# Performance work log

Measured on AMD Instinct MI355X. Metric: run time of the kernel, lower is better.

## Reference

```python
import jax, jax.numpy as jnp
import numpy as np

N_EXPERTS = 16
D_IN = 2048
D_OUT = 2048
BATCH = 4096


def setup_inputs() -> dict:
    key = jax.random.key(0)
    k_x, k_m, k_a, k_w, k_b = jax.random.split(key, 5)
    xs = jax.random.normal(k_x, (BATCH, D_IN), dtype=jnp.float32)
    mxs = jax.random.normal(k_m, (BATCH,), dtype=jnp.float32)
    actions = jax.random.randint(k_a, (BATCH,), 0, N_EXPERTS, dtype=jnp.int64)
    # Per-expert Linear params: W[e] is [d_out, d_in], b[e] is [d_out]
    scale = 1.0 / np.sqrt(D_IN)
    W = jax.random.uniform(k_w, (N_EXPERTS, D_OUT, D_IN), dtype=jnp.float32,
                           minval=-scale, maxval=scale)
    b = jax.random.uniform(k_b, (N_EXPERTS, D_OUT), dtype=jnp.float32,
                           minval=-scale, maxval=scale)
    return {"xs": xs, "mxs": mxs, "actions": actions, "W": W, "b": b}


def reference(xs, mxs, actions, W, b):
    # Original: per-sample dispatch y[i] = submodule[actions[i]](x[i]).
    # Grouped form: for each expert e, run the full-batch GEMM and combine
    # with a mask (fixed small loop over experts; no data-dim Python loop).
    ys = jnp.zeros((xs.shape[0], W.shape[1]), dtype=xs.dtype)
    for e in range(W.shape[0]):
        ye = xs @ W[e].T + b[e]                      # [B, d_out]
        mask = (actions == e)[:, None]               # [B, 1]
        ys = jnp.where(mask, ye, ys)
    return (ys, mxs, actions)
```

## Files before the change

kernel.cpp:

```cpp
#include <hip/hip_runtime.h>
#include <hip/hip_bf16.h>

#define BATCH 4096
#define NEXP  16
#define DIN   2048
#define DOUT  2048

#define BM 128
#define BN 64
#define NKT 64
#define NPAIR 32

#define WS_X_OFF   65536
#define PADROWS    4352
#define WS_X_BYTES ((size_t)PADROWS * 4096)

typedef __attribute__((ext_vector_type(4))) float f32x4;
typedef __attribute__((ext_vector_type(8))) short bf16x8;

__global__ void sort_kernel(const int* __restrict__ actions,
                            const float* __restrict__ mxs,
                            float* __restrict__ out_tail,
                            int* __restrict__ offs,
                            int* __restrict__ poffs,
                            int* __restrict__ sorted) {
    __shared__ int s_cnt[NEXP];
    __shared__ int s_cur[NEXP];
    const int tid = threadIdx.x;
    if (tid < NEXP) s_cnt[tid] = 0;
    __syncthreads();
    for (int i = tid; i < BATCH; i += blockDim.x) {
        int a = actions[i];
        atomicAdd(&s_cnt[a], 1);
        out_tail[i] = mxs[i];
        out_tail[BATCH + i] = (float)a;
    }
    __syncthreads();
    if (tid == 0) {
        int run = 0, prun = 0;
        for (int e = 0; e < NEXP; ++e) {
            offs[e] = run;  s_cur[e] = run;
            poffs[e] = prun;
            run += s_cnt[e];
            prun += (s_cnt[e] + 15) & ~15;
        }
        offs[NEXP] = run;
        poffs[NEXP] = prun;
    }
    __syncthreads();
    for (int i = tid; i < BATCH; i += blockDim.x) {
        int e = actions[i];
        int pos = atomicAdd(&s_cur[e], 1);
        sorted[pos] = i;
    }
}

__device__ __forceinline__ unsigned rne2(float x0, float x1) {
    unsigned b0 = __float_as_uint(x0), b1 = __float_as_uint(x1);
    b0 = b0 + 0x7FFFu + ((b0 >> 16) & 1u);
    b1 = b1 + 0x7FFFu + ((b1 >> 16) & 1u);
    return (b1 & 0xFFFF0000u) | (b0 >> 16);
}

__device__ __forceinline__ int lidxW(int r, int kb) {
    return r * 64 + ((kb ^ (r & 7)) << 3);
}

__device__ __forceinline__ int lidx(int r, int kb) {
    return r * 64 + ((kb ^ (r & 7)) << 3);
}

__global__ void xsplit_kernel(const float* __restrict__ xs,
                              const int* __restrict__ sorted,
                              const int* __restrict__ offs,
                              const int* __restrict__ poffs,
                              unsigned char* __restrict__ xws) {
    const int t = threadIdx.x;
    const int slot = t & 15;
    const int ktq = t >> 4;
    const int p = blockIdx.x * 16 + slot;
    if (p >= poffs[NEXP]) return;
    int e = 0;
#pragma unroll
    for (int i = 1; i < NEXP; ++i)
        if (p >= poffs[i]) e = i;
    const int local = p - poffs[e];
    if (local >= offs[e + 1] - offs[e]) return;
    const int src = sorted[offs[e] + local];
    const float* srow = xs + (size_t)src * DIN;
    unsigned char* gbase = xws + (size_t)blockIdx.x * 65536;
#pragma unroll
    for (int q = 0; q < 4; ++q) {
        const int kt = ktq * 4 + q;
        const float* s = srow + kt * 32;
        uint4 L[4];
#pragma unroll
        for (int j = 0; j < 4; ++j) {
            float4 a = *(const float4*)(s + 8 * j);
            float4 b = *(const float4*)(s + 8 * j + 4);
            L[j].x = rne2(a.x, a.y); L[j].y = rne2(a.z, a.w);
            L[j].z = rne2(b.x, b.y); L[j].w = rne2(b.z, b.w);
        }
        unsigned char* d = gbase + kt * 1024 + slot * 16;
#pragma unroll
        for (int g = 0; g < 4; ++g)
            *(uint4*)(d + g * 256) = L[g];
    }
}

__global__ __launch_bounds__(256, 3)
void gemm_kernel(const unsigned char* __restrict__ xws,
                 const float* __restrict__ W,
                 const float* __restrict__ bias,
                 const int* __restrict__ offs,
                 const int* __restrict__ poffs,
                 const int* __restrict__ sorted,
                 float* __restrict__ out) {
    __shared__ __align__(16) unsigned short Wl[2][BN * 64];

    const int e = blockIdx.y;
    const int start = offs[e];
    const int cnt = offs[e + 1] - start;
    const int m0 = blockIdx.z * BM;
    if (m0 >= cnt) return;
    const int n0 = blockIdx.x * BN;

    const int tid = threadIdx.x;
    const int lane = tid & 63;
    const int wave = tid >> 6;
    const int g = lane >> 4, rl = lane & 15;

    const int swr = tid >> 2;
    const int wkq = tid & 3;
    const float* wsrc = W + ((size_t)e * DOUT + n0 + swr) * DIN + wkq * 16;

    const unsigned char* xb[2];
#pragma unroll
    for (int mi = 0; mi < 2; ++mi) {
        int prow = poffs[e] + m0 + wave * 32 + mi * 16;
        if (prow > PADROWS - 16) prow = PADROWS - 16;
        xb[mi] = xws + ((size_t)prow >> 4) * 65536 + (size_t)lane * 16;
    }

    f32x4 acc[2][4];
#pragma unroll
    for (int i = 0; i < 2; ++i)
#pragma unroll
        for (int j = 0; j < 4; ++j) acc[i][j] = (f32x4){0.f, 0.f, 0.f, 0.f};

    float4 pwA[4], pwB[4];
#pragma unroll
    for (int j = 0; j < 4; ++j) pwA[j] = *(const float4*)(wsrc + 0 * 64 + 4 * j);
#pragma unroll
    for (int j = 0; j < 4; ++j) pwB[j] = *(const float4*)(wsrc + 1 * 64 + 4 * j);
    bf16x8 axA[2][2], axB[2][2];
#pragma unroll
    for (int mi = 0; mi < 2; ++mi) {
        axA[mi][0] = *(const bf16x8*)(xb[mi]);
        axA[mi][1] = *(const bf16x8*)(xb[mi] + 1024);
    }
    {
        uint4 u0, u1;
        u0.x = rne2(pwA[0].x, pwA[0].y); u0.y = rne2(pwA[0].z, pwA[0].w);
        u0.z = rne2(pwA[1].x, pwA[1].y); u0.w = rne2(pwA[1].z, pwA[1].w);
        u1.x = rne2(pwA[2].x, pwA[2].y); u1.y = rne2(pwA[2].z, pwA[2].w);
        u1.z = rne2(pwA[3].x, pwA[3].y); u1.w = rne2(pwA[3].z, pwA[3].w);
        *(uint4*)&Wl[0][lidxW(swr, 2 * wkq)]     = u0;
        *(uint4*)&Wl[0][lidxW(swr, 2 * wkq + 1)] = u1;
#pragma unroll
        for (int j = 0; j < 4; ++j) pwA[j] = *(const float4*)(wsrc + 2 * 64 + 4 * j);
    }

    int pr = 0;

#define KSTEP(AXC, AXN, PWU, PAR) do {                                         \
    __builtin_amdgcn_sched_barrier(0);                                         \
    asm volatile("s_waitcnt lgkmcnt(0)");                                      \
    __builtin_amdgcn_sched_barrier(0);                                         \
    __builtin_amdgcn_s_barrier();                                              \
    __builtin_amdgcn_sched_barrier(0);                                         \
    bf16x8 bh[2][4];                                                           \
    _Pragma("unroll")                                                          \
    for (int j = 0; j < 2; ++j)                                                \
        _Pragma("unroll")                                                      \
        for (int ni = 0; ni < 4; ++ni)                                         \
            bh[j][ni] = *(const bf16x8*)&Wl[PAR][lidxW(ni * 16 + rl, j * 4 + g)]; \
    {                   \
      int _kn = ((pr + 1) & (NPAIR - 1)) * 2;                                  \
      _Pragma("unroll")                                                        \
      for (int mi = 0; mi < 2; ++mi) {                                         \
          AXN[mi][0] = *(const bf16x8*)(xb[mi] + (size_t)_kn * 1024);          \
          AXN[mi][1] = *(const bf16x8*)(xb[mi] + (size_t)(_kn + 1) * 1024);    \
      } }                                                                      \
    {                      \
      uint4 u0, u1;                                                            \
      u0.x = rne2(PWU[0].x, PWU[0].y); u0.y = rne2(PWU[0].z, PWU[0].w);        \
      u0.z = rne2(PWU[1].x, PWU[1].y); u0.w = rne2(PWU[1].z, PWU[1].w);        \
      u1.x = rne2(PWU[2].x, PWU[2].y); u1.y = rne2(PWU[2].z, PWU[2].w);        \
      u1.z = rne2(PWU[3].x, PWU[3].y); u1.w = rne2(PWU[3].z, PWU[3].w);        \
      *(uint4*)&Wl[PAR ^ 1][lidxW(swr, 2 * wkq)]     = u0;                     \
      *(uint4*)&Wl[PAR ^ 1][lidxW(swr, 2 * wkq + 1)] = u1; }                   \
    {                                        \
      int _k3 = (pr + 3) & (NPAIR - 1);                                        \
      _Pragma("unroll")                                                        \
      for (int j = 0; j < 4; ++j)                                              \
          PWU[j] = *(const float4*)(wsrc + (size_t)_k3 * 64 + 4 * j); }        \
    __builtin_amdgcn_s_setprio(1);                                             \
    _Pragma("unroll")                                                          \
    for (int j = 0; j < 2; ++j)                                                \
        _Pragma("unroll")                                                      \
        for (int mi = 0; mi < 2; ++mi)                                         \
            _Pragma("unroll")                                                  \
            for (int ni = 0; ni < 4; ++ni)                                     \
                acc[mi][ni] = __builtin_amdgcn_mfma_f32_16x16x32_bf16(AXC[mi][j], bh[j][ni], acc[mi][ni], 0, 0, 0); \
    __builtin_amdgcn_s_setprio(0);                                             \
    ++pr;                                                                      \
} while (0)

#pragma unroll 1
    for (int it = 0; it < NPAIR / 2; ++it) {
        KSTEP(axA, axB, pwB, 0);
        KSTEP(axB, axA, pwA, 1);
    }
#undef KSTEP

    float bv[4];
#pragma unroll
    for (int ni = 0; ni < 4; ++ni)
        bv[ni] = bias[(size_t)e * DOUT + n0 + ni * 16 + rl];
#pragma unroll
    for (int mi = 0; mi < 2; ++mi) {
#pragma unroll
        for (int j = 0; j < 4; ++j) {
            int rm = m0 + wave * 32 + mi * 16 + g * 4 + j;
            if (rm < cnt) {
                int s = sorted[start + rm];
                float* orow = out + (size_t)s * DOUT + n0 + rl;
#pragma unroll
                for (int ni = 0; ni < 4; ++ni)
                    orow[ni * 16] = acc[mi][ni][j] + bv[ni];
            }
        }
    }
}

__device__ __forceinline__ void split_pair(float x0, float x1, unsigned& h, unsigned& l) {
    unsigned b0 = __float_as_uint(x0), b1 = __float_as_uint(x1);
    unsigned h0 = b0 & 0xFFFF0000u;
    unsigned h1 = b1 & 0xFFFF0000u;
    h = h1 | (b0 >> 16);
    unsigned l0 = __float_as_uint(x0 - __uint_as_float(h0));
    unsigned l1 = __float_as_uint(x1 - __uint_as_float(h1));
    l = (l1 & 0xFFFF0000u) | (l0 >> 16);
}
__device__ __forceinline__ void split_f4pair(float4 a, float4 b, uint4& h, uint4& l) {
    split_pair(a.x, a.y, h.x, l.x);
    split_pair(a.z, a.w, h.y, l.y);
    split_pair(b.x, b.y, h.z, l.z);
    split_pair(b.z, b.w, h.w, l.w);
}

__global__ __launch_bounds__(256, 3)
void gemm_fb(const float* __restrict__ xs,
             const float* __restrict__ W,
             const float* __restrict__ bias,
             const int* __restrict__ offs,
             const int* __restrict__ sorted,
             float* __restrict__ out) {
    __shared__ __align__(16) unsigned short Xs[128 * 64];
    __shared__ __align__(16) unsigned short Ws[64 * 64];

    const int e = blockIdx.y;
    const int start = offs[e];
    const int cnt = offs[e + 1] - start;
    const int m0 = blockIdx.z * 128;
    if (m0 >= cnt) return;
    const int n0 = blockIdx.x * 64;

    const int tid = threadIdx.x;
    const int lane = tid & 63;
    const int wave = tid >> 6;
    const int wm = wave >> 1, wn = wave & 1;
    const int srow = tid & 127, kq = tid >> 7;
    const int swr = tid >> 2, wkq = tid & 3;

    const int rm_s = m0 + srow;
    const int xrow = (rm_s < cnt) ? sorted[start + rm_s] : -1;
    const float* xsrc = xs + (size_t)(xrow < 0 ? 0 : xrow) * DIN + kq * 16;
    const float* wsrc = W + ((size_t)e * DOUT + n0 + swr) * DIN + wkq * 8;

    f32x4 acc[4][2];
#pragma unroll
    for (int i = 0; i < 4; ++i)
#pragma unroll
        for (int j = 0; j < 2; ++j) acc[i][j] = (f32x4){0.f, 0.f, 0.f, 0.f};

    float4 px[4], pw[2];
#pragma unroll
    for (int j = 0; j < 4; ++j)
        px[j] = (xrow >= 0) ? *(const float4*)(xsrc + j * 4) : make_float4(0.f, 0.f, 0.f, 0.f);
    pw[0] = *(const float4*)(wsrc);
    pw[1] = *(const float4*)(wsrc + 4);

    for (int k0 = 0; k0 < DIN; k0 += 32) {
        {
            uint4 xh0, xl0, xh1, xl1, wh, wl;
            split_f4pair(px[0], px[1], xh0, xl0);
            split_f4pair(px[2], px[3], xh1, xl1);
            split_f4pair(pw[0], pw[1], wh, wl);
            *(uint4*)&Xs[lidx(srow, 2 * kq)]         = xh0;
            *(uint4*)&Xs[lidx(srow, 2 * kq + 1)]     = xh1;
            *(uint4*)&Xs[lidx(srow, 4 + 2 * kq)]     = xl0;
            *(uint4*)&Xs[lidx(srow, 4 + 2 * kq + 1)] = xl1;
            *(uint4*)&Ws[lidx(swr, wkq)]             = wh;
            *(uint4*)&Ws[lidx(swr, 4 + wkq)]         = wl;
        }
        __syncthreads();
        {
            int kn = (k0 + 32 < DIN) ? (k0 + 32) : 0;
#pragma unroll
            for (int j = 0; j < 4; ++j)
                px[j] = (xrow >= 0) ? *(const float4*)(xsrc + kn + j * 4) : make_float4(0.f, 0.f, 0.f, 0.f);
            pw[0] = *(const float4*)(wsrc + kn);
            pw[1] = *(const float4*)(wsrc + kn + 4);
        }
        {
            const int gg = lane >> 4, rrl = lane & 15;
            bf16x8 ah[4], al[4], bh[2], bl[2];
#pragma unroll
            for (int mi = 0; mi < 4; ++mi) {
                int R = wm * 64 + mi * 16 + rrl;
                ah[mi] = *(const bf16x8*)&Xs[lidx(R, gg)];
                al[mi] = *(const bf16x8*)&Xs[lidx(R, 4 + gg)];
            }
#pragma unroll
            for (int ni = 0; ni < 2; ++ni) {
                int R = wn * 32 + ni * 16 + rrl;
                bh[ni] = *(const bf16x8*)&Ws[lidx(R, gg)];
                bl[ni] = *(const bf16x8*)&Ws[lidx(R, 4 + gg)];
            }
#pragma unroll
            for (int mi = 0; mi < 4; ++mi)
#pragma unroll
                for (int ni = 0; ni < 2; ++ni)
                    acc[mi][ni] = __builtin_amdgcn_mfma_f32_16x16x32_bf16(ah[mi], bh[ni], acc[mi][ni], 0, 0, 0);
#pragma unroll
            for (int mi = 0; mi < 4; ++mi)
#pragma unroll
                for (int ni = 0; ni < 2; ++ni)
                    acc[mi][ni] = __builtin_amdgcn_mfma_f32_16x16x32_bf16(ah[mi], bl[ni], acc[mi][ni], 0, 0, 0);
#pragma unroll
            for (int mi = 0; mi < 4; ++mi)
#pragma unroll
                for (int ni = 0; ni < 2; ++ni)
                    acc[mi][ni] = __builtin_amdgcn_mfma_f32_16x16x32_bf16(al[mi], bh[ni], acc[mi][ni], 0, 0, 0);
        }
        __syncthreads();
    }

    const int gg = lane >> 4, rrl = lane & 15;
    float bv[2];
#pragma unroll
    for (int ni = 0; ni < 2; ++ni)
        bv[ni] = bias[(size_t)e * DOUT + n0 + wn * 32 + ni * 16 + rrl];
#pragma unroll
    for (int mi = 0; mi < 4; ++mi) {
#pragma unroll
        for (int j = 0; j < 4; ++j) {
            int rm = m0 + wm * 64 + mi * 16 + gg * 4 + j;
            if (rm < cnt) {
                int s = sorted[start + rm];
                float* orow = out + (size_t)s * DOUT + n0 + wn * 32 + rrl;
#pragma unroll
                for (int ni = 0; ni < 2; ++ni)
                    orow[ni * 16] = acc[mi][ni][j] + bv[ni];
            }
        }
    }
}

extern "C" void kernel_launch(void* const* d_in, const int* in_sizes, int n_in,
                              void* d_out, int out_size, void* d_ws, size_t ws_size,
                              hipStream_t stream) {
    const float* xs      = (const float*)d_in[0];
    const float* mxs     = (const float*)d_in[1];
    const int*   actions = (const int*)d_in[2];
    const float* W       = (const float*)d_in[3];
    const float* b       = (const float*)d_in[4];
    float* out = (float*)d_out;

    int* ws_i   = (int*)d_ws;
    int* offs   = ws_i;
    int* poffs  = ws_i + 20;
    int* sorted = ws_i + 64;

    sort_kernel<<<1, 1024, 0, stream>>>(actions, mxs,
                                        out + (size_t)BATCH * DOUT,
                                        offs, poffs, sorted);

    if (ws_size >= WS_X_OFF + WS_X_BYTES) {
        unsigned char* xws = (unsigned char*)d_ws + WS_X_OFF;
        xsplit_kernel<<<PADROWS / 16, 256, 0, stream>>>(xs, sorted, offs, poffs, xws);
        dim3 grid(DOUT / BN, NEXP, BATCH / BM);
        gemm_kernel<<<grid, 256, 0, stream>>>(xws, W, b, offs, poffs, sorted, out);
    } else {
        dim3 grid(DOUT / 64, NEXP, BATCH / 128);
        gemm_fb<<<grid, 256, 0, stream>>>(xs, W, b, offs, sorted, out);
    }
}
```

Measured before the change: 163.9 us.

## Pre-convert W to bf16 fragment layout and run LDS-free direct-load GEMM

Adds a wsplit kernel that converts all expert weights to bf16 in the MFMA-fragment tiled layout inside the workspace. A new GEMM then loads both X and W fragments straight from global memory into registers, double-buffered, with no LDS staging and no barriers. This removes the per-block fp32-to-bf16 conversion of W and the LDS round trip. In exchange it adds a full pass over the 256MB weight tensor every call, and the path needs a large workspace (the old LDS kernel remains as the fallback). It also drops the split-precision fallback kernel.

Result: slower. 205.7 us (+25.6%).

```diff
diff --git a/kernel.cpp b/kernel.cpp
--- a/kernel.cpp
+++ b/kernel.cpp
@@ -14,6 +14,10 @@
 #define WS_X_OFF   65536
 #define PADROWS    4352
 #define WS_X_BYTES ((size_t)PADROWS * 4096)
+#define WS_W_OFF   (WS_X_OFF + WS_X_BYTES)
+#define WS_W_BYTES ((size_t)NEXP * 128 * 65536)
+#define NEED_ALL   (WS_W_OFF + WS_W_BYTES)
+#define NEED_X     (WS_X_OFF + WS_X_BYTES)
 
 typedef __attribute__((ext_vector_type(4))) float f32x4;
 typedef __attribute__((ext_vector_type(8))) short bf16x8;
@@ -66,10 +70,6 @@
     return r * 64 + ((kb ^ (r & 7)) << 3);
 }
 
-__device__ __forceinline__ int lidx(int r, int kb) {
-    return r * 64 + ((kb ^ (r & 7)) << 3);
-}
-
 __global__ void xsplit_kernel(const float* __restrict__ xs,
                               const int* __restrict__ sorted,
                               const int* __restrict__ offs,
@@ -108,14 +108,143 @@
     }
 }
 
+__global__ void wsplit_kernel(const float* __restrict__ W,
+                              unsigned char* __restrict__ wws) {
+    const int t = threadIdx.x;
+    const int slot = t & 15;
+    const int ktq = t >> 4;
+    const int gw = blockIdx.x;
+    const float* srow = W + ((size_t)gw * 16 + slot) * DIN;
+    unsigned char* gbase = wws + (size_t)gw * 65536;
+#pragma unroll
+    for (int q = 0; q < 4; ++q) {
+        const int kt = ktq * 4 + q;
+        const float* s = srow + kt * 32;
+        uint4 L[4];
+#pragma unroll
+        for (int j = 0; j < 4; ++j) {
+            float4 a = *(const float4*)(s + 8 * j);
+            float4 b = *(const float4*)(s + 8 * j + 4);
+            L[j].x = rne2(a.x, a.y); L[j].y = rne2(a.z, a.w);
+            L[j].z = rne2(b.x, b.y); L[j].w = rne2(b.z, b.w);
+        }
+        unsigned char* d = gbase + kt * 1024 + slot * 16;
+#pragma unroll
+        for (int g = 0; g < 4; ++g)
+            *(uint4*)(d + g * 256) = L[g];
+    }
+}
+
 __global__ __launch_bounds__(256, 3)
-void gemm_kernel(const unsigned char* __restrict__ xws,
-                 const float* __restrict__ W,
+void gemm_direct(const unsigned char* __restrict__ xws,
+                 const unsigned char* __restrict__ wws,
                  const float* __restrict__ bias,
                  const int* __restrict__ offs,
                  const int* __restrict__ poffs,
                  const int* __restrict__ sorted,
                  float* __restrict__ out) {
+    const int e = blockIdx.y;
+    const int start = offs[e];
+    const int cnt = offs[e + 1] - start;
+    const int m0 = blockIdx.z * BM;
+    if (m0 >= cnt) return;
+    const int n0 = blockIdx.x * BN;
+
+    const int tid = threadIdx.x;
+    const int lane = tid & 63;
+    const int wave = tid >> 6;
+    const int g = lane >> 4, rl = lane & 15;
+
+    const unsigned char* ab[2];
+#pragma unroll
+    for (int mi = 0; mi < 2; ++mi) {
+        int prow = poffs[e] + m0 + wave * 32 + mi * 16;
+        if (prow > PADROWS - 16) prow = PADROWS - 16;
+        ab[mi] = xws + ((size_t)prow >> 4) * 65536 + (size_t)lane * 16;
+    }
+    const unsigned char* bb[4];
+#pragma unroll
+    for (int ni = 0; ni < 4; ++ni)
+        bb[ni] = wws + ((size_t)(e * 128 + (n0 >> 4) + ni)) * 65536
+                     + (size_t)lane * 16;
+
+    f32x4 acc[2][4];
+#pragma unroll
+    for (int i = 0; i < 2; ++i)
+#pragma unroll
+        for (int j = 0; j < 4; ++j) acc[i][j] = (f32x4){0.f, 0.f, 0.f, 0.f};
+
+    bf16x8 aA[2][2], aB[2][2];
+    bf16x8 bA[2][4], bB[2][4];
+
+#define LOADP(AX, BX, P) do {                                                  \
+    const size_t _o = (size_t)(P) * 2048;                                      \
+    _Pragma("unroll")                                                          \
+    for (int _mi = 0; _mi < 2; ++_mi) {                                        \
+        AX[_mi][0] = *(const bf16x8*)(ab[_mi] + _o);                           \
+        AX[_mi][1] = *(const bf16x8*)(ab[_mi] + _o + 1024);                    \
+    }                                                                          \
+    _Pragma("unroll")                                                          \
+    for (int _ni = 0; _ni < 4; ++_ni) {                                        \
+        BX[0][_ni] = *(const bf16x8*)(bb[_ni] + _o);                           \
+        BX[1][_ni] = *(const bf16x8*)(bb[_ni] + _o + 1024);                    \
+    }                                                                          \
+} while (0)
+
+#define DOMFMA(AX, BX) do {                                                    \
+    __builtin_amdgcn_s_setprio(1);                                             \
+    _Pragma("unroll")                                                          \
+    for (int _j = 0; _j < 2; ++_j)                                             \
+        _Pragma("unroll")                                                      \
+        for (int _mi = 0; _mi < 2; ++_mi)                                      \
+            _Pragma("unroll")                                                  \
+            for (int _ni = 0; _ni < 4; ++_ni)                                  \
+                acc[_mi][_ni] = __builtin_amdgcn_mfma_f32_16x16x32_bf16(       \
+                    AX[_mi][_j], BX[_j][_ni], acc[_mi][_ni], 0, 0, 0);         \
+    __builtin_amdgcn_s_setprio(0);                                             \
+} while (0)
+
+    LOADP(aA, bA, 0);
+    int pr = 0;
+#pragma unroll 1
+    for (int it = 0; it < NPAIR / 2; ++it) {
+        LOADP(aB, bB, pr + 1);
+        DOMFMA(aA, bA);
+        LOADP(aA, bA, (pr + 2) & (NPAIR - 1));
+        DOMFMA(aB, bB);
+        pr += 2;
+    }
+#undef LOADP
+#undef DOMFMA
+
+    float bv[4];
+#pragma unroll
+    for (int ni = 0; ni < 4; ++ni)
+        bv[ni] = bias[(size_t)e * DOUT + n0 + ni * 16 + rl];
+#pragma unroll
+    for (int mi = 0; mi < 2; ++mi) {
+#pragma unroll
+        for (int j = 0; j < 4; ++j) {
+            int rm = m0 + wave * 32 + mi * 16 + g * 4 + j;
+            if (rm < cnt) {
+                int s = sorted[start + rm];
+                float* orow = out + (size_t)s * DOUT + n0 + rl;
+#pragma unroll
+                for (int ni = 0; ni < 4; ++ni)
+                    orow[ni * 16] = acc[mi][ni][j] + bv[ni];
+            }
+        }
+    }
+}
+
+__global__ __launch_bounds__(256, 3)
+void gemm_lds(const unsigned char* __restrict__ xws,
+              const float* __restrict__ W,
+              const float* __restrict__ bias,
+              const int* __restrict__ offs,
+              const int* __restrict__ poffs,
+              const int* __restrict__ sorted,
+              float* __restrict__ out) {
     __shared__ __align__(16) unsigned short Wl[2][BN * 64];
 
     const int e = blockIdx.y;
@@ -185,23 +314,20 @@
         _Pragma("unroll")                                                      \
         for (int ni = 0; ni < 4; ++ni)                                         \
             bh[j][ni] = *(const bf16x8*)&Wl[PAR][lidxW(ni * 16 + rl, j * 4 + g)]; \
-    {                   \
-      int _kn = ((pr + 1) & (NPAIR - 1)) * 2;                                  \
+    { int _kn = ((pr + 1) & (NPAIR - 1)) * 2;                                  \
       _Pragma("unroll")                                                        \
       for (int mi = 0; mi < 2; ++mi) {                                         \
           AXN[mi][0] = *(const bf16x8*)(xb[mi] + (size_t)_kn * 1024);          \
           AXN[mi][1] = *(const bf16x8*)(xb[mi] + (size_t)(_kn + 1) * 1024);    \
       } }                                                                      \
-    {                      \
-      uint4 u0, u1;                                                            \
+    { uint4 u0, u1;                                                            \
       u0.x = rne2(PWU[0].x, PWU[0].y); u0.y = rne2(PWU[0].z, PWU[0].w);        \
       u0.z = rne2(PWU[1].x, PWU[1].y); u0.w = rne2(PWU[1].z, PWU[1].w);        \
       u1.x = rne2(PWU[2].x, PWU[2].y); u1.y = rne2(PWU[2].z, PWU[2].w);        \
       u1.z = rne2(PWU[3].x, PWU[3].y); u1.w = rne2(PWU[3].z, PWU[3].w);        \
       *(uint4*)&Wl[PAR ^ 1][lidxW(swr, 2 * wkq)]     = u0;                     \
       *(uint4*)&Wl[PAR ^ 1][lidxW(swr, 2 * wkq + 1)] = u1; }                   \
-    {                                        \
-      int _k3 = (pr + 3) & (NPAIR - 1);                                        \
+    { int _k3 = (pr + 3) & (NPAIR - 1);                                        \
       _Pragma("unroll")                                                        \
       for (int j = 0; j < 4; ++j)                                              \
           PWU[j] = *(const float4*)(wsrc + (size_t)_k3 * 64 + 4 * j); }        \
@@ -244,141 +370,6 @@
     }
 }
 
-__device__ __forceinline__ void split_pair(float x0, float x1, unsigned& h, unsigned& l) {
-    unsigned b0 = __float_as_uint(x0), b1 = __float_as_uint(x1);
-    unsigned h0 = b0 & 0xFFFF0000u;
-    unsigned h1 = b1 & 0xFFFF0000u;
-    h = h1 | (b0 >> 16);
-    unsigned l0 = __float_as_uint(x0 - __uint_as_float(h0));
-    unsigned l1 = __float_as_uint(x1 - __uint_as_float(h1));
-    l = (l1 & 0xFFFF0000u) | (l0 >> 16);
-}
-__device__ __forceinline__ void split_f4pair(float4 a, float4 b, uint4& h, uint4& l) {
-    split_pair(a.x, a.y, h.x, l.x);
-    split_pair(a.z, a.w, h.y, l.y);
-    split_pair(b.x, b.y, h.z, l.z);
-    split_pair(b.z, b.w, h.w, l.w);
-}
-
-__global__ __launch_bounds__(256, 3)
-void gemm_fb(const float* __restrict__ xs,
-             const float* __restrict__ W,
-             const float* __restrict__ bias,
-             const int* __restrict__ offs,
-             const int* __restrict__ sorted,
-             float* __restrict__ out) {
-    __shared__ __align__(16) unsigned short Xs[128 * 64];
-    __shared__ __align__(16) unsigned short Ws[64 * 64];
-
-    const int e = blockIdx.y;
-    const int start = offs[e];
-    const int cnt = offs[e + 1] - start;
-    const int m0 = blockIdx.z * 128;
-    if (m0 >= cnt) return;
-    const int n0 = blockIdx.x * 64;
-
-    const int tid = threadIdx.x;
-    const int lane = tid & 63;
-    const int wave = tid >> 6;
-    const int wm = wave >> 1, wn = wave & 1;
-    const int srow = tid & 127, kq = tid >> 7;
-    const int swr = tid >> 2, wkq = tid & 3;
-
-    const int rm_s = m0 + srow;
-    const int xrow = (rm_s < cnt) ? sorted[start + rm_s] : -1;
-    const float* xsrc = xs + (size_t)(xrow < 0 ? 0 : xrow) * DIN + kq * 16;
-    const float* wsrc = W + ((size_t)e * DOUT + n0 + swr) * DIN + wkq * 8;
-
-    f32x4 acc[4][2];
-#pragma unroll
-    for (int i = 0; i < 4; ++i)
-#pragma unroll
-        for (int j = 0; j < 2; ++j) acc[i][j] = (f32x4){0.f, 0.f, 0.f, 0.f};
-
-    float4 px[4], pw[2];
-#pragma unroll
-    for (int j = 0; j < 4; ++j)
-        px[j] = (xrow >= 0) ? *(const float4*)(xsrc + j * 4) : make_float4(0.f, 0.f, 0.f, 0.f);
-    pw[0] = *(const float4*)(wsrc);
-    pw[1] = *(const float4*)(wsrc + 4);
-
-    for (int k0 = 0; k0 < DIN; k0 += 32) {
-        {
-            uint4 xh0, xl0, xh1, xl1, wh, wl;
-            split_f4pair(px[0], px[1], xh0, xl0);
-            split_f4pair(px[2], px[3], xh1, xl1);
-            split_f4pair(pw[0], pw[1], wh, wl);
-            *(uint4*)&Xs[lidx(srow, 2 * kq)]         = xh0;
-            *(uint4*)&Xs[lidx(srow, 2 * kq + 1)]     = xh1;
-            *(uint4*)&Xs[lidx(srow, 4 + 2 * kq)]     = xl0;
-            *(uint4*)&Xs[lidx(srow, 4 + 2 * kq + 1)] = xl1;
-            *(uint4*)&Ws[lidx(swr, wkq)]             = wh;
-            *(uint4*)&Ws[lidx(swr, 4 + wkq)]         = wl;
-        }
-        __syncthreads();
-        {
-            int kn = (k0 + 32 < DIN) ? (k0 + 32) : 0;
-#pragma unroll
-            for (int j = 0; j < 4; ++j)
-                px[j] = (xrow >= 0) ? *(const float4*)(xsrc + kn + j * 4) : make_float4(0.f, 0.f, 0.f, 0.f);
-            pw[0] = *(const float4*)(wsrc + kn);
-            pw[1] = *(const float4*)(wsrc + kn + 4);
-        }
-        {
-            const int gg = lane >> 4, rrl = lane & 15;
-            bf16x8 ah[4], al[4], bh[2], bl[2];
-#pragma unroll
-            for (int mi = 0; mi < 4; ++mi) {
-                int R = wm * 64 + mi * 16 + rrl;
-                ah[mi] = *(const bf16x8*)&Xs[lidx(R, gg)];
-                al[mi] = *(const bf16x8*)&Xs[lidx(R, 4 + gg)];
-            }
-#pragma unroll
-            for (int ni = 0; ni < 2; ++ni) {
-                int R = wn * 32 + ni * 16 + rrl;
-                bh[ni] = *(const bf16x8*)&Ws[lidx(R, gg)];
-                bl[ni] = *(const bf16x8*)&Ws[lidx(R, 4 + gg)];
-            }
-#pragma unroll
-            for (int mi = 0; mi < 4; ++mi)
-#pragma unroll
-                for (int ni = 0; ni < 2; ++ni)
-                    acc[mi][ni] = __builtin_amdgcn_mfma_f32_16x16x32_bf16(ah[mi], bh[ni], acc[mi][ni], 0, 0, 0);
-#pragma unroll
-            for (int mi = 0; mi < 4; ++mi)
-#pragma unroll
-                for (int ni = 0; ni < 2; ++ni)
-                    acc[mi][ni] = __builtin_amdgcn_mfma_f32_16x16x32_bf16(ah[mi], bl[ni], acc[mi][ni], 0, 0, 0);
-#pragma unroll
-            for (int mi = 0; mi < 4; ++mi)
-#pragma unroll
-                for (int ni = 0; ni < 2; ++ni)
-                    acc[mi][ni] = __builtin_amdgcn_mfma_f32_16x16x32_bf16(al[mi], bh[ni], acc[mi][ni], 0, 0, 0);
-        }
-        __syncthreads();
-    }
-
-    const int gg = lane >> 4, rrl = lane & 15;
-    float bv[2];
-#pragma unroll
-    for (int ni = 0; ni < 2; ++ni)
-        bv[ni] = bias[(size_t)e * DOUT + n0 + wn * 32 + ni * 16 + rrl];
-#pragma unroll
-    for (int mi = 0; mi < 4; ++mi) {
-#pragma unroll
-        for (int j = 0; j < 4; ++j) {
-            int rm = m0 + wm * 64 + mi * 16 + gg * 4 + j;
-            if (rm < cnt) {
-                int s = sorted[start + rm];
-                float* orow = out + (size_t)s * DOUT + n0 + wn * 32 + rrl;
-#pragma unroll
-                for (int ni = 0; ni < 2; ++ni)
-                    orow[ni * 16] = acc[mi][ni][j] + bv[ni];
-            }
-        }
-    }
-}
-
 extern "C" void kernel_launch(void* const* d_in, const int* in_sizes, int n_in,
                               void* d_out, int out_size, void* d_ws, size_t ws_size,
                               hipStream_t stream) {
@@ -398,13 +389,16 @@
                                         out + (size_t)BATCH * DOUT,
                                         offs, poffs, sorted);
 
-    if (ws_size >= WS_X_OFF + WS_X_BYTES) {
-        unsigned char* xws = (unsigned char*)d_ws + WS_X_OFF;
+    unsigned char* xws = (unsigned char*)d_ws + WS_X_OFF;
+    if (ws_size >= NEED_ALL) {
+        unsigned char* wws = (unsigned char*)d_ws + WS_W_OFF;
+        xsplit_kernel<<<PADROWS / 16, 256, 0, stream>>>(xs, sorted, offs, poffs, xws);
+        wsplit_kernel<<<NEXP * 128, 256, 0, stream>>>(W, wws);
+        dim3 grid(DOUT / BN, NEXP, BATCH / BM);
+        gemm_direct<<<grid, 256, 0, stream>>>(xws, wws, b, offs, poffs, sorted, out);
+    } else {
         xsplit_kernel<<<PADROWS / 16, 256, 0, stream>>>(xs, sorted, offs, poffs, xws);
         dim3 grid(DOUT / BN, NEXP, BATCH / BM);
-        gemm_kernel<<<grid, 256, 0, stream>>>(xws, W, b, offs, poffs, sorted, out);
-    } else {
-        dim3 grid(DOUT / 64, NEXP, BATCH / 128);
-        gemm_fb<<<grid, 256, 0, stream>>>(xs, W, b, offs, sorted, out);
-    }
-}
+        gemm_lds<<<grid, 256, 0, stream>>>(xws, W, b, offs, poffs, sorted, out);
+    }
+}
```
